# Kernel tuning notes

Measured on AMD Instinct MI355X. Metric: run time of the kernel, lower is better.

## Reference

```python
import jax, jax.numpy as jnp
import numpy as np

L, H, C, HS, V, BS = 4, 4, 1024, 256, 32000, 1024  # layers, heads, n_embd, head_size, vocab, block_size
B, T = 4, 1024
EPS = 1e-5

def _ln(x, g, b):
    mu = jnp.mean(x, axis=-1, keepdims=True)
    var = jnp.mean((x - mu) ** 2, axis=-1, keepdims=True)
    return (x - mu) / jnp.sqrt(var + EPS) * g + b

def setup_inputs() -> dict:
    key = jax.random.key(0)
    ks = iter(jax.random.split(key, 32))
    s = 0.02
    inp = {
        'idx': jax.random.randint(next(ks), (B, T), 0, V),
        'tok_emb': jax.random.normal(next(ks), (V, C), jnp.float32) * s,
        'pos_emb': jax.random.normal(next(ks), (BS, C), jnp.float32) * s,
        'wq': jax.random.normal(next(ks), (L, H, C, HS), jnp.float32) * s,
        'wk': jax.random.normal(next(ks), (L, H, C, HS), jnp.float32) * s,
        'wv': jax.random.normal(next(ks), (L, H, C, HS), jnp.float32) * s,
        'proj_w': jax.random.normal(next(ks), (L, C, C), jnp.float32) * s,
        'proj_b': jnp.zeros((L, C), jnp.float32),
        'ln1_g': jnp.ones((L, C), jnp.float32),
        'ln1_b': jnp.zeros((L, C), jnp.float32),
        'ln2_g': jnp.ones((L, C), jnp.float32),
        'ln2_b': jnp.zeros((L, C), jnp.float32),
        'ff_w1': jax.random.normal(next(ks), (L, C, 4 * C), jnp.float32) * s,
        'ff_b1': jnp.zeros((L, 4 * C), jnp.float32),
        'ff_w2': jax.random.normal(next(ks), (L, 4 * C, C), jnp.float32) * s,
        'ff_b2': jnp.zeros((L, C), jnp.float32),
        'lnf_g': jnp.ones((C,), jnp.float32),
        'lnf_b': jnp.zeros((C,), jnp.float32),
        'head_w': jax.random.normal(next(ks), (C, V), jnp.float32) * s,
        'head_b': jnp.zeros((V,), jnp.float32),
    }
    return inp

def reference(idx, tok_emb, pos_emb, wq, wk, wv, proj_w, proj_b, ln1_g, ln1_b,
              ln2_g, ln2_b, ff_w1, ff_b1, ff_w2, ff_b2, lnf_g, lnf_b, head_w, head_b):
    b, t = idx.shape
    x = tok_emb[idx] + pos_emb[:t]  # (B,T,C)
    causal = jnp.tril(jnp.ones((t, t), bool))
    inv_sqrt_c = np.float32(1.0 / np.sqrt(C))  # NOTE: original scales by sqrt(n_embd), not head_size
    for l in range(L):
        xn = _ln(x, ln1_g[l], ln1_b[l])
        q = jnp.einsum('btc,hcd->bhtd', xn, wq[l])
        k = jnp.einsum('bsc,hcd->bhsd', xn, wk[l])
        v = jnp.einsum('bsc,hcd->bhsd', xn, wv[l])
        scores = jnp.einsum('bhtd,bhsd->bhts', q, k)
        scores = jnp.where(causal, scores, -jnp.inf) * inv_sqrt_c
        # original: F.softmax(xdot, dim=1) on (B,T,T) -> normalize over the QUERY axis
        alpha = jax.nn.softmax(scores, axis=2)
        y = jnp.einsum('bhts,bhsd->bhtd', alpha, v)
        y = y.transpose(0, 2, 1, 3).reshape(b, t, C)  # concat heads
        x = x + y @ proj_w[l] + proj_b[l]
        xn2 = _ln(x, ln2_g[l], ln2_b[l])
        h = jax.nn.relu(xn2 @ ff_w1[l] + ff_b1[l])
        x = x + h @ ff_w2[l] + ff_b2[l]
    x = _ln(x, lnf_g, lnf_b)
    logits = x @ head_w + head_b  # (B,T,V)
    return logits
```

## Files before the change

### kernel.cpp

```cpp
#include <hip/hip_runtime.h>


#define C_  1024
#define T_  1024
#define HS_ 256
#define H_  4
#define L_  4
#define V_  32000
#define B_  4
#define M_  4096

typedef __attribute__((ext_vector_type(8))) short  bfx8;
typedef __attribute__((ext_vector_type(4))) float  fx4;
typedef __attribute__((ext_vector_type(4))) unsigned short usx4;
typedef __attribute__((ext_vector_type(8))) unsigned short usx8;

__device__ __forceinline__ unsigned short f2bf(float f) {
  unsigned int u = __builtin_bit_cast(unsigned int, f);
  u += 0x7fffu + ((u >> 16) & 1u);
  return (unsigned short)(u >> 16);
}
__device__ __forceinline__ float bf2f(unsigned short u) {
  return __builtin_bit_cast(float, ((unsigned int)u) << 16);
}

__device__ __forceinline__ void gload16(const unsigned short* g, unsigned short* l) {
  __builtin_amdgcn_global_load_lds(
      (const __attribute__((address_space(1))) unsigned int*)g,
      (__attribute__((address_space(3))) unsigned int*)l, 16, 0, 0);
}

__device__ __forceinline__ void xcd_swz(int& bx, int& by, int& bz) {
  const int gx = gridDim.x, gy = gridDim.y;
  const int nwg = gx * gy * gridDim.z;
  if (nwg & 7) return;
  int lin = (bz * gy + by) * gx + bx;
  lin = (lin & 7) * (nwg >> 3) + (lin >> 3);
  bx = lin % gx; lin /= gx; by = lin % gy; bz = lin / gy;
}

template<int BIAS, int RES, int RELU, int OUTBF>
__global__ __launch_bounds__(256, 2) void gemm_bf16(
    const unsigned short* __restrict__ A, const unsigned short* __restrict__ Bm,
    const float* __restrict__ bias, const float* __restrict__ res,
    void* __restrict__ out,
    int M, int N, int K, int lda, int ldb, int ldc,
    long sA, long sB, long sC1, long sC2, int zShift, long rowOuter)
{
  __shared__ unsigned short As[128 * 32];
  __shared__ unsigned short Bs[128 * 32];
  int bx = blockIdx.x, by = blockIdx.y, bz = blockIdx.z;
  xcd_swz(bx, by, bz);
  const int z = bz;
  A  += (long)z * sA;
  Bm += (long)z * sB;
  const long outOff = ((long)(z >> zShift)) * sC1 + (long)(z & ((1 << zShift) - 1)) * sC2;
  const int m0 = bx * 128, n0 = by * 128;
  const int tid = threadIdx.x;
  const int lane = tid & 63, wave = tid >> 6;
  const int wm = (wave >> 1) * 64, wn = (wave & 1) * 64;
  const int fr = lane & 15, kb = lane >> 4;
  const int sr = lane >> 2;
  const int csw = (((lane & 3) ^ ((lane >> 3) & 3)) << 3);
  const int aco = ((kb ^ ((lane >> 1) & 3)) << 3);

  fx4 acc[4][4] = {};

  for (int k0 = 0; k0 < K; k0 += 32) {
    #pragma unroll
    for (int i = 0; i < 2; ++i) {
      const int c = wave * 2 + i;
      gload16(A  + (long)(m0 + c * 16 + sr) * lda + k0 + csw, &As[c * 512]);
      gload16(Bm + (long)(n0 + c * 16 + sr) * ldb + k0 + csw, &Bs[c * 512]);
    }
    __syncthreads();
    bfx8 af[4], bf[4];
    #pragma unroll
    for (int i = 0; i < 4; ++i)
      af[i] = *reinterpret_cast<const bfx8*>(&As[(wm + i * 16 + fr) * 32 + aco]);
    #pragma unroll
    for (int j = 0; j < 4; ++j)
      bf[j] = *reinterpret_cast<const bfx8*>(&Bs[(wn + j * 16 + fr) * 32 + aco]);
    #pragma unroll
    for (int i = 0; i < 4; ++i)
      #pragma unroll
      for (int j = 0; j < 4; ++j)
        acc[i][j] = __builtin_amdgcn_mfma_f32_16x16x32_bf16(af[i], bf[j], acc[i][j], 0, 0, 0);
    __syncthreads();
  }

  const float* resp = res;
  if (RES) resp += outOff;
  const int rbase = (lane >> 4) * 4;
  #pragma unroll
  for (int j = 0; j < 4; ++j) {
    const int n = n0 + wn + j * 16 + fr;
    float bv = 0.f;
    if (BIAS) bv = bias[n];
    #pragma unroll
    for (int i = 0; i < 4; ++i) {
      #pragma unroll
      for (int r = 0; r < 4; ++r) {
        const int m = m0 + wm + i * 16 + rbase + r;
        const long off = outOff + ((long)(m >> 10)) * rowOuter + (long)(m & 1023) * ldc + n;
        float val = acc[i][j][r] + bv;
        if (RELU) val = fmaxf(val, 0.f);
        if (RES) val += resp[((long)(m >> 10)) * rowOuter + (long)(m & 1023) * ldc + n];
        if (OUTBF) ((unsigned short*)out)[off] = f2bf(val);
        else       ((float*)out)[off] = val;
      }
    }
  }
}

#define BAR() __builtin_amdgcn_s_barrier()
#define LGKM() { asm volatile("s_waitcnt lgkmcnt(0)" ::: "memory"); \
                 __builtin_amdgcn_sched_barrier(0); }
#define VM8()  asm volatile("s_waitcnt vmcnt(8)" ::: "memory")
#define STA(tau, kh) { const int tc = (tau) < NT ? (tau) : NT - 1; \
  const unsigned short* src = A + (long)(m0 + wave * 16 + srow) * lda + tc * 64 + (kh) * 32 + csw; \
  unsigned short* d = &S[(((tau) & 1) * 2 + (kh)) * 8192 + wave * 512]; \
  gload16(src, d); gload16(src + (long)128 * lda, d + 4096); }
#define STB(tau, kh) { const int tc = (tau) < NT ? (tau) : NT - 1; \
  const unsigned short* src = Bm + (long)(n0 + wave * 16 + srow) * ldb + tc * 64 + (kh) * 32 + csw; \
  unsigned short* d = &S[32768 + (((tau) & 1) * 2 + (kh)) * 8192 + wave * 512]; \
  gload16(src, d); gload16(src + (long)128 * ldb, d + 4096); }
#define RDA(dst, par, kh, rh) { _Pragma("unroll") for (int i = 0; i < 4; ++i) \
  dst[i] = *reinterpret_cast<const bfx8*>(&S[((par)*2+(kh))*8192 + (wr*128 + (rh)*64 + i*16 + fr)*32 + aco]); }
#define RDB(dst, par, kh) { _Pragma("unroll") for (int j = 0; j < 4; ++j) \
  dst[j] = *reinterpret_cast<const bfx8*>(&S[32768 + ((par)*2+(kh))*8192 + (wc*64 + j*16 + fr)*32 + aco]); }
#define MM(rh, afx, bfx) { __builtin_amdgcn_s_setprio(1); \
  _Pragma("unroll") for (int i = 0; i < 4; ++i) { _Pragma("unroll") for (int j = 0; j < 4; ++j) \
    acc[(rh)*4+i][j] = __builtin_amdgcn_mfma_f32_16x16x32_bf16(afx[i], bfx[j], acc[(rh)*4+i][j], 0, 0, 0); } \
  __builtin_amdgcn_s_setprio(0); }

template<int BIAS, int RELU, int OUTBF, int EPI>
__global__ __launch_bounds__(512, 2) void gemm256(
    const unsigned short* __restrict__ A, const unsigned short* __restrict__ Bm,
    const float* __restrict__ bias, void* __restrict__ out,
    int K, int lda, int ldb, int ldc, long sA, long sB, long sC1)
{
  __shared__ unsigned short S[65536];
  int bx = blockIdx.x, by = blockIdx.y, bz = blockIdx.z;
  xcd_swz(bx, by, bz);
  const int z = bz;
  A  += (long)z * sA;
  Bm += (long)z * sB;
  const long outOff = (long)z * sC1;
  const int m0 = bx * 256, n0 = by * 256;
  const int tid = threadIdx.x;
  const int lane = tid & 63, wave = tid >> 6;
  const int wr = wave >> 2, wc = wave & 3;
  const int fr = lane & 15, kb = lane >> 4;
  const int srow = lane >> 2;
  const int csw = (((lane & 3) ^ (((lane >> 5) & 1) << 1)) << 3);
  const int aco = ((kb ^ (((fr >> 3) & 1) << 1)) << 3);
  const int NT = K >> 6;
  const int NI = NT >> 1;

  fx4 acc[8][4] = {};
  bfx8 afa[4], afb[4], bf0[4], bf1[4];

  STB(0, 0); STA(0, 0); STB(0, 1); STA(0, 1);
  STB(1, 0); STA(1, 0); STB(1, 1); STA(1, 1);
  VM8();
  BAR();
  RDA(afa, 0, 0, 0); RDB(bf1, 0, 0);
  LGKM();
  BAR();

  for (int t = 0; t < NI; ++t) {
    const int u = 2 * t;
    STB(u + 2, 0); RDA(afb, 0, 0, 1);                 MM(0, afa, bf1); LGKM(); BAR();
    STA(u + 2, 0); RDA(afa, 0, 1, 0); RDB(bf0, 0, 1); MM(1, afb, bf1); LGKM(); VM8(); BAR();
    STB(u + 2, 1); RDA(afb, 0, 1, 1);                 MM(0, afa, bf0); LGKM(); BAR();
    STA(u + 2, 1); RDA(afa, 1, 0, 0); RDB(bf1, 1, 0); MM(1, afb, bf0); LGKM(); VM8(); BAR();
    STB(u + 3, 0); RDA(afb, 1, 0, 1);                 MM(0, afa, bf1); LGKM(); BAR();
    STA(u + 3, 0); RDA(afa, 1, 1, 0); RDB(bf0, 1, 1); MM(1, afb, bf1); LGKM(); VM8(); BAR();
    STB(u + 3, 1); RDA(afb, 1, 1, 1);                 MM(0, afa, bf0); LGKM(); BAR();
    STA(u + 3, 1); RDA(afa, 0, 0, 0); RDB(bf1, 0, 0); MM(1, afb, bf0); LGKM(); VM8(); BAR();
  }
  asm volatile("s_waitcnt vmcnt(0)" ::: "memory");
  BAR();

  const int rbase = (lane >> 4) * 4;
  unsigned short* dst1 = nullptr;
  if (EPI == 1) {
    const int sel = n0 >> 10, h = (n0 >> 8) & 3;
    const int bq = m0 >> 10, tq0 = m0 & 1023;
    dst1 = (unsigned short*)out + ((long)sel * B_ + bq) * H_ * T_ * HS_
         + (long)h * T_ * HS_ + (long)tq0 * HS_;
  }
  float* lf = (float*)S;
  #pragma unroll
  for (int jh = 0; jh < 2; ++jh) {
    #pragma unroll
    for (int jj = 0; jj < 2; ++jj)
      #pragma unroll
      for (int i = 0; i < 8; ++i)
        #pragma unroll
        for (int r = 0; r < 4; ++r) {
          const int row = i * 16 + rbase + r;
          const int cw = (jj * 16 + fr) ^ ((row & 7) << 2);
          lf[wave * 4096 + row * 32 + cw] = acc[i][jh * 2 + jj][r];
        }
    #pragma unroll
    for (int rs = 0; rs < 16; ++rs) {
      const int row = rs * 8 + (lane >> 3);
      const int c0 = (lane & 7) * 4;
      const int cw = c0 ^ ((row & 7) << 2);
      fx4 val = *reinterpret_cast<const fx4*>(&lf[wave * 4096 + row * 32 + cw]);
      const int nl = wc * 64 + jh * 32 + c0;
      if (BIAS) {
        const float4 bb = *reinterpret_cast<const float4*>(bias + n0 + nl);
        val[0] += bb.x; val[1] += bb.y; val[2] += bb.z; val[3] += bb.w;
      }
      if (RELU) {
        val[0] = fmaxf(val[0], 0.f); val[1] = fmaxf(val[1], 0.f);
        val[2] = fmaxf(val[2], 0.f); val[3] = fmaxf(val[3], 0.f);
      }
      if (EPI == 1) {
        const long off = (long)(wr * 128 + row) * HS_ + nl;
        usx4 o = { f2bf(val[0]), f2bf(val[1]), f2bf(val[2]), f2bf(val[3]) };
        *reinterpret_cast<usx4*>(dst1 + off) = o;
      } else {
        const long off = outOff + (long)(m0 + wr * 128 + row) * ldc + n0 + nl;
        if (OUTBF) {
          usx4 o = { f2bf(val[0]), f2bf(val[1]), f2bf(val[2]), f2bf(val[3]) };
          *reinterpret_cast<usx4*>((unsigned short*)out + off) = o;
        } else {
          __builtin_nontemporal_store(val, reinterpret_cast<fx4*>((float*)out + off));
        }
      }
    }
    __builtin_amdgcn_sched_barrier(0);
  }
}

template<typename TIN>
__global__ __launch_bounds__(256) void transpose_k(const TIN* __restrict__ src,
    unsigned short* __restrict__ dst, int R, int Cc, int zShiftT, long sOuter) {
  __shared__ float ts[64][65];
  const long zb = blockIdx.z;
  src += zb * (long)R * Cc;
  dst += (zb >> zShiftT) * sOuter + (zb & ((1 << zShiftT) - 1)) * ((long)R * Cc);
  const int r0 = blockIdx.y * 64, c0 = blockIdx.x * 64;
  const int tr = threadIdx.x >> 4;
  const int tc = (threadIdx.x & 15) * 4;
  #pragma unroll
  for (int it = 0; it < 4; ++it) {
    const int r = tr + it * 16;
    float4 v;
    if constexpr (sizeof(TIN) == 4) {
      v = *reinterpret_cast<const float4*>(src + (long)(r0 + r) * Cc + c0 + tc);
    } else {
      usx4 u = *reinterpret_cast<const usx4*>(src + (long)(r0 + r) * Cc + c0 + tc);
      v.x = bf2f(u[0]); v.y = bf2f(u[1]); v.z = bf2f(u[2]); v.w = bf2f(u[3]);
    }
    ts[r][tc + 0] = v.x; ts[r][tc + 1] = v.y; ts[r][tc + 2] = v.z; ts[r][tc + 3] = v.w;
  }
  __syncthreads();
  #pragma unroll
  for (int it = 0; it < 4; ++it) {
    const int cj = tr + it * 16;
    usx4 o = { f2bf(ts[tc + 0][cj]), f2bf(ts[tc + 1][cj]),
               f2bf(ts[tc + 2][cj]), f2bf(ts[tc + 3][cj]) };
    *reinterpret_cast<usx4*>(dst + (long)(c0 + cj) * R + r0 + tc) = o;
  }
}

__global__ __launch_bounds__(256) void embed_k(const int* __restrict__ idx,
                                               const float* __restrict__ tok,
                                               const float* __restrict__ pos,
                                               float* __restrict__ x) {
  const int row = blockIdx.x;
  const int t = row & (T_ - 1);
  const int id = idx[row];
  const int c = threadIdx.x * 4;
  const float4 a = *reinterpret_cast<const float4*>(tok + (long)id * C_ + c);
  const float4 p = *reinterpret_cast<const float4*>(pos + (long)t * C_ + c);
  float4 ov = { a.x + p.x, a.y + p.y, a.z + p.z, a.w + p.w };
  *reinterpret_cast<float4*>(x + (long)row * C_ + c) = ov;
}

__global__ __launch_bounds__(256) void ln_k(const float* __restrict__ x,
                                            const float* __restrict__ g,
                                            const float* __restrict__ b,
                                            unsigned short* __restrict__ o) {
  __shared__ float red[8];
  const int row = blockIdx.x;
  const int c = threadIdx.x * 4;
  const float4 v = *reinterpret_cast<const float4*>(x + (long)row * C_ + c);
  float s1 = v.x + v.y + v.z + v.w;
  float s2 = v.x * v.x + v.y * v.y + v.z * v.z + v.w * v.w;
  #pragma unroll
  for (int off = 32; off; off >>= 1) {
    s1 += __shfl_xor(s1, off, 64);
    s2 += __shfl_xor(s2, off, 64);
  }
  const int lane = threadIdx.x & 63, w = threadIdx.x >> 6;
  if (lane == 0) { red[w] = s1; red[4 + w] = s2; }
  __syncthreads();
  s1 = red[0] + red[1] + red[2] + red[3];
  s2 = red[4] + red[5] + red[6] + red[7];
  const float mu = s1 * (1.f / C_);
  float var = s2 * (1.f / C_) - mu * mu;
  var = fmaxf(var, 0.f);
  const float inv = rsqrtf(var + 1e-5f);
  const float4 gg = *reinterpret_cast<const float4*>(g + c);
  const float4 bb = *reinterpret_cast<const float4*>(b + c);
  usx4 ov;
  ov[0] = f2bf((v.x - mu) * inv * gg.x + bb.x);
  ov[1] = f2bf((v.y - mu) * inv * gg.y + bb.y);
  ov[2] = f2bf((v.z - mu) * inv * gg.z + bb.z);
  ov[3] = f2bf((v.w - mu) * inv * gg.w + bb.w);
  *reinterpret_cast<usx4*>(o + (long)row * C_ + c) = ov;
}

__global__ __launch_bounds__(256) void colsmT_k(const unsigned short* __restrict__ sc,
                                                unsigned short* __restrict__ alpha) {
  __shared__ float invs[64];
  __shared__ float tile[64][65];
  const int z = blockIdx.z;
  const int s0 = blockIdx.x * 64;
  const int r = threadIdx.x >> 2;
  const int tq = threadIdx.x & 3;
  const int s = s0 + r;
  const unsigned short* p = sc + (long)z * T_ * T_ + (long)s * T_ + tq * 256;
  const float scale = 0.03125f;

  float zsum = 0.f;
  for (int i = 0; i < 32; ++i) {
    const usx8 u = *reinterpret_cast<const usx8*>(p + i * 8);
    #pragma unroll
    for (int j = 0; j < 8; ++j) {
      const int t = tq * 256 + i * 8 + j;
      if (t >= s) zsum += __expf(bf2f(u[j]) * scale);
    }
  }
  zsum += __shfl_xor(zsum, 1, 64);
  zsum += __shfl_xor(zsum, 2, 64);
  if (tq == 0) invs[r] = 1.f / zsum;
  __syncthreads();
  const float inv = invs[r];

  const unsigned short* prow = sc + (long)z * T_ * T_ + (long)s * T_;
  unsigned short* ob = alpha + (long)z * T_ * T_ + s0;
  const int wrow = threadIdx.x >> 2;
  const int seg  = threadIdx.x & 3;
  for (int tc = 0; tc < 16; ++tc) {
    #pragma unroll
    for (int half = 0; half < 2; ++half) {
      const int tb = tc * 64 + tq * 16 + half * 8;
      const usx8 u = *reinterpret_cast<const usx8*>(prow + tb);
      #pragma unroll
      for (int j = 0; j < 8; ++j) {
        const int t = tb + j;
        const float a = (t >= s) ? __expf(bf2f(u[j]) * scale) * inv : 0.f;
        tile[tq * 16 + half * 8 + j][r] = a;
      }
    }
    __syncthreads();
    usx8 o0, o1;
    #pragma unroll
    for (int k = 0; k < 8; ++k) o0[k] = f2bf(tile[wrow][seg * 16 + k]);
    #pragma unroll
    for (int k = 0; k < 8; ++k) o1[k] = f2bf(tile[wrow][seg * 16 + 8 + k]);
    unsigned short* od = ob + (long)(tc * 64 + wrow) * T_ + seg * 16;
    *reinterpret_cast<usx8*>(od) = o0;
    *reinterpret_cast<usx8*>(od + 8) = o1;
    __syncthreads();
  }
}

extern "C" void kernel_launch(void* const* d_in, const int* in_sizes, int n_in,
                              void* d_out, int out_size, void* d_ws, size_t ws_size,
                              hipStream_t stream) {
  const int*   idx    = (const int*)d_in[0];
  const float* tok    = (const float*)d_in[1];
  const float* pos    = (const float*)d_in[2];
  const float* wq     = (const float*)d_in[3];
  const float* wk     = (const float*)d_in[4];
  const float* wv     = (const float*)d_in[5];
  const float* proj_w = (const float*)d_in[6];
  const float* proj_b = (const float*)d_in[7];
  const float* ln1_g  = (const float*)d_in[8];
  const float* ln1_b  = (const float*)d_in[9];
  const float* ln2_g  = (const float*)d_in[10];
  const float* ln2_b  = (const float*)d_in[11];
  const float* ff_w1  = (const float*)d_in[12];
  const float* ff_b1  = (const float*)d_in[13];
  const float* ff_w2  = (const float*)d_in[14];
  const float* ff_b2  = (const float*)d_in[15];
  const float* lnf_g  = (const float*)d_in[16];
  const float* lnf_b  = (const float*)d_in[17];
  const float* head_w = (const float*)d_in[18];
  const float* head_b = (const float*)d_in[19];
  float* outp = (float*)d_out;

  typedef unsigned short us;
  char* w = (char*)d_ws;
  float* x    = (float*)(w + 0);
  us* xn      = (us*)(w + 16777216);
  us* qkv     = (us*)(w + 25165824);
  us* kptr    = qkv + 4194304;
  us* vptr    = qkv + 8388608;
  us* vT      = (us*)(w + 50331648);
  us* yc      = (us*)(w + 58720256);
  us* sc      = (us*)(w + 67108864);
  us* headT   = (us*)(w + 67108864);
  us* alpha   = (us*)(w + 100663296);
  us* hidden  = (us*)(w + 134217728);
  us* wqkvT   = (us*)(w + 167772160);
  us* projT   = (us*)(w + 192937984);
  us* ff1T    = (us*)(w + 201326592);
  us* ff2T    = (us*)(w + 234881024);
  if (ws_size < (size_t)268435456) return;

  const long HHC = (long)H_ * HS_ * C_;
  transpose_k<float><<<dim3(HS_/64, C_/64, L_*H_), 256, 0, stream>>>(wq, wqkvT,           C_, HS_, 2, 3*HHC);
  transpose_k<float><<<dim3(HS_/64, C_/64, L_*H_), 256, 0, stream>>>(wk, wqkvT + HHC,     C_, HS_, 2, 3*HHC);
  transpose_k<float><<<dim3(HS_/64, C_/64, L_*H_), 256, 0, stream>>>(wv, wqkvT + 2*HHC,   C_, HS_, 2, 3*HHC);
  transpose_k<float><<<dim3(C_/64, C_/64, L_), 256, 0, stream>>>(proj_w, projT, C_, C_, 0, (long)C_*C_);
  transpose_k<float><<<dim3(4*C_/64, C_/64, L_), 256, 0, stream>>>(ff_w1, ff1T, C_, 4*C_, 0, (long)C_*4*C_);
  transpose_k<float><<<dim3(C_/64, 4*C_/64, L_), 256, 0, stream>>>(ff_w2, ff2T, 4*C_, C_, 0, (long)4*C_*C_);

  embed_k<<<M_, 256, 0, stream>>>(idx, tok, pos, x);

  for (int l = 0; l < L_; ++l) {
    ln_k<<<M_, 256, 0, stream>>>(x, ln1_g + l * C_, ln1_b + l * C_, xn);

    dim3 gqkv(M_/256, 3*C_/256, 1);
    gemm256<0,0,1,1><<<gqkv, 512, 0, stream>>>(xn, wqkvT + l * 3 * HHC, nullptr, qkv,
        C_, C_, C_, 0, 0, 0, 0);

    dim3 gs(T_/256, T_/256, B_*H_);
    gemm256<0,0,1,0><<<gs, 512, 0, stream>>>(kptr, qkv, nullptr, sc,
        HS_, HS_, HS_, T_, (long)T_*HS_, (long)T_*HS_, (long)T_*T_);

    colsmT_k<<<dim3(T_/64, 1, B_*H_), 256, 0, stream>>>(sc, alpha);

    transpose_k<us><<<dim3(HS_/64, T_/64, B_*H_), 256, 0, stream>>>(vptr, vT, T_, HS_, 0, (long)T_*HS_);

    dim3 gp(T_/128, HS_/128, B_*H_);
    gemm_bf16<0,0,0,1><<<gp, 256, 0, stream>>>(alpha, vT, nullptr, nullptr, yc,
        T_, HS_, T_, T_, T_, C_, (long)T_*T_, (long)HS_*T_, (long)T_*C_, HS_, 2, (long)T_*C_);

    dim3 gj(M_/128, C_/128, 1);
    gemm_bf16<1,1,0,0><<<gj, 256, 0, stream>>>(yc, projT + (long)l*C_*C_, proj_b + l*C_, x, x,
        M_, C_, C_, C_, C_, C_, 0, 0, 0, 0, 0, (long)T_*C_);

    ln_k<<<M_, 256, 0, stream>>>(x, ln2_g + l * C_, ln2_b + l * C_, xn);

    dim3 g1(M_/256, 4*C_/256, 1);
    gemm256<1,1,1,0><<<g1, 512, 0, stream>>>(xn, ff1T + (long)l*4*C_*C_, ff_b1 + (long)l*4*C_,
        hidden, C_, C_, C_, 4*C_, 0, 0, 0);

    dim3 g2(M_/128, C_/128, 1);
    gemm_bf16<1,1,0,0><<<g2, 256, 0, stream>>>(hidden, ff2T + (long)l*C_*4*C_, ff_b2 + l*C_, x, x,
        M_, C_, 4*C_, 4*C_, 4*C_, C_, 0, 0, 0, 0, 0, (long)T_*C_);
  }

  ln_k<<<M_, 256, 0, stream>>>(x, lnf_g, lnf_b, xn);

  transpose_k<float><<<dim3(V_/64, C_/64, 1), 256, 0, stream>>>(head_w, headT, C_, V_, 0, (long)C_*V_);

  dim3 gh(M_/256, V_/256, 1);
  gemm256<1,0,0,0><<<gh, 512, 0, stream>>>(xn, headT, head_b, outp,
      C_, C_, C_, V_, 0, 0, 0);
}
```

Baseline: 1.619 ms.

## Skip masked causal tiles, restructure gemm256 main loop, drop XCD swizzle

```diff
diff --git a/kernel.cpp b/kernel.cpp
--- a/kernel.cpp
+++ b/kernel.cpp
@@ -30,16 +30,7 @@
       (__attribute__((address_space(3))) unsigned int*)l, 16, 0, 0);
 }
 
-__device__ __forceinline__ void xcd_swz(int& bx, int& by, int& bz) {
-  const int gx = gridDim.x, gy = gridDim.y;
-  const int nwg = gx * gy * gridDim.z;
-  if (nwg & 7) return;
-  int lin = (bz * gy + by) * gx + bx;
-  lin = (lin & 7) * (nwg >> 3) + (lin >> 3);
-  bx = lin % gx; lin /= gx; by = lin % gy; bz = lin / gy;
-}
-
-template<int BIAS, int RES, int RELU, int OUTBF>
+template<int BIAS, int RES, int RELU, int OUTBF, int TRI>
 __global__ __launch_bounds__(256, 2) void gemm_bf16(
     const unsigned short* __restrict__ A, const unsigned short* __restrict__ Bm,
     const float* __restrict__ bias, const float* __restrict__ res,
@@ -49,13 +40,12 @@
 {
   __shared__ unsigned short As[128 * 32];
   __shared__ unsigned short Bs[128 * 32];
-  int bx = blockIdx.x, by = blockIdx.y, bz = blockIdx.z;
-  xcd_swz(bx, by, bz);
-  const int z = bz;
+  const int z = blockIdx.z;
   A  += (long)z * sA;
   Bm += (long)z * sB;
   const long outOff = ((long)(z >> zShift)) * sC1 + (long)(z & ((1 << zShift) - 1)) * sC2;
-  const int m0 = bx * 128, n0 = by * 128;
+  const int m0 = blockIdx.x * 128, n0 = blockIdx.y * 128;
+  if (TRI) K = min(K, m0 + 128);
   const int tid = threadIdx.x;
   const int lane = tid & 63, wave = tid >> 6;
   const int wm = (wave >> 1) * 64, wn = (wave & 1) * 64;
@@ -125,29 +115,28 @@
   const unsigned short* src = Bm + (long)(n0 + wave * 16 + srow) * ldb + tc * 64 + (kh) * 32 + csw; \
   unsigned short* d = &S[32768 + (((tau) & 1) * 2 + (kh)) * 8192 + wave * 512]; \
   gload16(src, d); gload16(src + (long)128 * ldb, d + 4096); }
-#define RDA(dst, par, kh, rh) { _Pragma("unroll") for (int i = 0; i < 4; ++i) \
-  dst[i] = *reinterpret_cast<const bfx8*>(&S[((par)*2+(kh))*8192 + (wr*128 + (rh)*64 + i*16 + fr)*32 + aco]); }
+#define RDA8(dst, par, kh) { _Pragma("unroll") for (int i = 0; i < 8; ++i) \
+  dst[i] = *reinterpret_cast<const bfx8*>(&S[((par)*2+(kh))*8192 + (wr*128 + i*16 + fr)*32 + aco]); }
 #define RDB(dst, par, kh) { _Pragma("unroll") for (int j = 0; j < 4; ++j) \
   dst[j] = *reinterpret_cast<const bfx8*>(&S[32768 + ((par)*2+(kh))*8192 + (wc*64 + j*16 + fr)*32 + aco]); }
-#define MM(rh, afx, bfx) { __builtin_amdgcn_s_setprio(1); \
-  _Pragma("unroll") for (int i = 0; i < 4; ++i) { _Pragma("unroll") for (int j = 0; j < 4; ++j) \
-    acc[(rh)*4+i][j] = __builtin_amdgcn_mfma_f32_16x16x32_bf16(afx[i], bfx[j], acc[(rh)*4+i][j], 0, 0, 0); } \
+#define MM32(afx, bfx) { __builtin_amdgcn_s_setprio(1); \
+  _Pragma("unroll") for (int i = 0; i < 8; ++i) { _Pragma("unroll") for (int j = 0; j < 4; ++j) \
+    acc[i][j] = __builtin_amdgcn_mfma_f32_16x16x32_bf16(afx[i], bfx[j], acc[i][j], 0, 0, 0); } \
   __builtin_amdgcn_s_setprio(0); }
 
-template<int BIAS, int RELU, int OUTBF, int EPI>
+template<int BIAS, int RELU, int OUTBF, int EPI, int TRI>
 __global__ __launch_bounds__(512, 2) void gemm256(
     const unsigned short* __restrict__ A, const unsigned short* __restrict__ Bm,
     const float* __restrict__ bias, void* __restrict__ out,
     int K, int lda, int ldb, int ldc, long sA, long sB, long sC1)
 {
   __shared__ unsigned short S[65536];
-  int bx = blockIdx.x, by = blockIdx.y, bz = blockIdx.z;
-  xcd_swz(bx, by, bz);
-  const int z = bz;
+  if (TRI && blockIdx.y < blockIdx.x) return;
+  const int z = blockIdx.z;
   A  += (long)z * sA;
   Bm += (long)z * sB;
   const long outOff = (long)z * sC1;
-  const int m0 = bx * 256, n0 = by * 256;
+  const int m0 = blockIdx.x * 256, n0 = blockIdx.y * 256;
   const int tid = threadIdx.x;
   const int lane = tid & 63, wave = tid >> 6;
   const int wr = wave >> 2, wc = wave & 3;
@@ -156,29 +145,27 @@
   const int csw = (((lane & 3) ^ (((lane >> 5) & 1) << 1)) << 3);
   const int aco = ((kb ^ (((fr >> 3) & 1) << 1)) << 3);
   const int NT = K >> 6;
-  const int NI = NT >> 1;
+  const int NK4 = K >> 7;
 
   fx4 acc[8][4] = {};
-  bfx8 afa[4], afb[4], bf0[4], bf1[4];
+  bfx8 afa[8], afb[8], bfa[4], bfb[4];
 
   STB(0, 0); STA(0, 0); STB(0, 1); STA(0, 1);
   STB(1, 0); STA(1, 0); STB(1, 1); STA(1, 1);
-  VM8();
-  BAR();
-  RDA(afa, 0, 0, 0); RDB(bf1, 0, 0);
-  LGKM();
-  BAR();
-
-  for (int t = 0; t < NI; ++t) {
+  VM8(); BAR();
+  RDA8(afa, 0, 0); RDB(bfa, 0, 0);
+  LGKM(); BAR();
+
+  for (int t = 0; t < NK4; ++t) {
     const int u = 2 * t;
-    STB(u + 2, 0); RDA(afb, 0, 0, 1);                 MM(0, afa, bf1); LGKM(); BAR();
-    STA(u + 2, 0); RDA(afa, 0, 1, 0); RDB(bf0, 0, 1); MM(1, afb, bf1); LGKM(); VM8(); BAR();
-    STB(u + 2, 1); RDA(afb, 0, 1, 1);                 MM(0, afa, bf0); LGKM(); BAR();
-    STA(u + 2, 1); RDA(afa, 1, 0, 0); RDB(bf1, 1, 0); MM(1, afb, bf0); LGKM(); VM8(); BAR();
-    STB(u + 3, 0); RDA(afb, 1, 0, 1);                 MM(0, afa, bf1); LGKM(); BAR();
-    STA(u + 3, 0); RDA(afa, 1, 1, 0); RDB(bf0, 1, 1); MM(1, afb, bf1); LGKM(); VM8(); BAR();
-    STB(u + 3, 1); RDA(afb, 1, 1, 1);                 MM(0, afa, bf0); LGKM(); BAR();
-    STA(u + 3, 1); RDA(afa, 0, 0, 0); RDB(bf1, 0, 0); MM(1, afb, bf0); LGKM(); VM8(); BAR();
+    STA(u + 2, 0); STB(u + 2, 0); RDA8(afb, 0, 1); RDB(bfb, 0, 1);
+    MM32(afa, bfa); LGKM(); VM8(); BAR();
+    STA(u + 2, 1); STB(u + 2, 1); RDA8(afa, 1, 0); RDB(bfa, 1, 0);
+    MM32(afb, bfb); LGKM(); VM8(); BAR();
+    STA(u + 3, 0); STB(u + 3, 0); RDA8(afb, 1, 1); RDB(bfb, 1, 1);
+    MM32(afa, bfa); LGKM(); VM8(); BAR();
+    STA(u + 3, 1); STB(u + 3, 1); RDA8(afa, 0, 0); RDB(bfa, 0, 0);
+    MM32(afb, bfb); LGKM(); VM8(); BAR();
   }
   asm volatile("s_waitcnt vmcnt(0)" ::: "memory");
   BAR();
@@ -431,11 +418,11 @@
     ln_k<<<M_, 256, 0, stream>>>(x, ln1_g + l * C_, ln1_b + l * C_, xn);
 
     dim3 gqkv(M_/256, 3*C_/256, 1);
-    gemm256<0,0,1,1><<<gqkv, 512, 0, stream>>>(xn, wqkvT + l * 3 * HHC, nullptr, qkv,
+    gemm256<0,0,1,1,0><<<gqkv, 512, 0, stream>>>(xn, wqkvT + l * 3 * HHC, nullptr, qkv,
         C_, C_, C_, 0, 0, 0, 0);
 
     dim3 gs(T_/256, T_/256, B_*H_);
-    gemm256<0,0,1,0><<<gs, 512, 0, stream>>>(kptr, qkv, nullptr, sc,
+    gemm256<0,0,1,0,1><<<gs, 512, 0, stream>>>(kptr, qkv, nullptr, sc,
         HS_, HS_, HS_, T_, (long)T_*HS_, (long)T_*HS_, (long)T_*T_);
 
     colsmT_k<<<dim3(T_/64, 1, B_*H_), 256, 0, stream>>>(sc, alpha);
@@ -443,21 +430,21 @@
     transpose_k<us><<<dim3(HS_/64, T_/64, B_*H_), 256, 0, stream>>>(vptr, vT, T_, HS_, 0, (long)T_*HS_);
 
     dim3 gp(T_/128, HS_/128, B_*H_);
-    gemm_bf16<0,0,0,1><<<gp, 256, 0, stream>>>(alpha, vT, nullptr, nullptr, yc,
+    gemm_bf16<0,0,0,1,1><<<gp, 256, 0, stream>>>(alpha, vT, nullptr, nullptr, yc,
         T_, HS_, T_, T_, T_, C_, (long)T_*T_, (long)HS_*T_, (long)T_*C_, HS_, 2, (long)T_*C_);
 
     dim3 gj(M_/128, C_/128, 1);
-    gemm_bf16<1,1,0,0><<<gj, 256, 0, stream>>>(yc, projT + (long)l*C_*C_, proj_b + l*C_, x, x,
+    gemm_bf16<1,1,0,0,0><<<gj, 256, 0, stream>>>(yc, projT + (long)l*C_*C_, proj_b + l*C_, x, x,
         M_, C_, C_, C_, C_, C_, 0, 0, 0, 0, 0, (long)T_*C_);
 
     ln_k<<<M_, 256, 0, stream>>>(x, ln2_g + l * C_, ln2_b + l * C_, xn);
 
     dim3 g1(M_/256, 4*C_/256, 1);
-    gemm256<1,1,1,0><<<g1, 512, 0, stream>>>(xn, ff1T + (long)l*4*C_*C_, ff_b1 + (long)l*4*C_,
+    gemm256<1,1,1,0,0><<<g1, 512, 0, stream>>>(xn, ff1T + (long)l*4*C_*C_, ff_b1 + (long)l*4*C_,
         hidden, C_, C_, C_, 4*C_, 0, 0, 0);
 
     dim3 g2(M_/128, C_/128, 1);
-    gemm_bf16<1,1,0,0><<<g2, 256, 0, stream>>>(hidden, ff2T + (long)l*C_*4*C_, ff_b2 + l*C_, x, x,
+    gemm_bf16<1,1,0,0,0><<<g2, 256, 0, stream>>>(hidden, ff2T + (long)l*C_*4*C_, ff_b2 + l*C_, x, x,
         M_, C_, 4*C_, 4*C_, 4*C_, C_, 0, 0, 0, 0, 0, (long)T_*C_);
   }
 
@@ -466,6 +453,6 @@
   transpose_k<float><<<dim3(V_/64, C_/64, 1), 256, 0, stream>>>(head_w, headT, C_, V_, 0, (long)C_*V_);
 
   dim3 gh(M_/256, V_/256, 1);
-  gemm256<1,0,0,0><<<gh, 512, 0, stream>>>(xn, headT, head_b, outp,
+  gemm256<1,0,0,0,0><<<gh, 512, 0, stream>>>(xn, headT, head_b, outp,
       C_, C_, C_, V_, 0, 0, 0);
 }
```

Result: slower. 1.850 ms (+14.2%).
